# Kernel tuning notes

Hardware: AMD Instinct MI355X
Metric: run time of the kernel (lower is better)

## Reference

```python
import jax, jax.numpy as jnp
import numpy as np
import math

B, M, DM = 4, 4096, 1024
H, HD = 16, 64            # head_dim = hidden_dim // num_heads
SEG, DIL = 128, 2         # segment_size, dilation_rate
BLOCK_M = 64              # kernel query-block size (min(64, M))
SCALE = HD ** -0.5


def _hilbert_map(seq_len):
    # Faithful port of create_hilbert_mapping_fixed (boustrophedon scan).
    if seq_len <= 64:
        return np.arange(seq_len, dtype=np.int32)
    g = int(math.ceil(math.sqrt(seq_len)))
    mp = np.zeros(seq_len, dtype=np.int64)
    idx = 0
    for row in range(g):
        cols = range(g) if row % 2 == 0 else range(g - 1, -1, -1)
        for col in cols:
            if idx < seq_len:
                lp = row * g + col
                if lp < seq_len:
                    mp[lp] = idx
                    idx += 1
    for i in range(seq_len):
        if i >= idx:
            mp[i] = i
    return mp.astype(np.int32)


def setup_inputs() -> dict:
    key = jax.random.key(0)
    k1, k2, k3 = jax.random.split(key, 3)
    x = jax.random.normal(k1, (B, M, DM), jnp.float32)
    Wqkv = jax.random.normal(k2, (3 * DM, DM), jnp.float32) * 0.02
    Wout = jax.random.normal(k3, (DM, DM), jnp.float32) * 0.02
    hmap = jnp.asarray(_hilbert_map(M))
    return {"x": x, "Wqkv": Wqkv, "Wout": Wout, "hmap": hmap}


def _hilbert_attention(x, Wqkv, Wout, hmap):
    Bn, Mn, _ = x.shape
    qkv = x @ Wqkv.T                                   # [B,M,3*DM]
    qkv = qkv.reshape(Bn, Mn, 3, H, HD).transpose(2, 0, 3, 1, 4)
    q, k, v = qkv[0], qkv[1], qkv[2]                   # [B,H,M,HD]

    S = Mn // SEG           # number of segments
    T = SEG // DIL          # keys per segment (dilated offsets 0, DIL, 2*DIL, ...)
    NB = SEG // BLOCK_M     # query blocks per segment

    # Queries gathered through Hilbert map, pre-scaled (as in kernel).
    qh = q[:, :, hmap, :] * SCALE                      # [B,H,M,HD]

    # Dilated key positions per segment, gathered through Hilbert map.
    key_pos = (jnp.arange(S)[:, None] * SEG + jnp.arange(T)[None, :] * DIL).reshape(-1)
    kh = k[:, :, hmap[key_pos], :].reshape(Bn, H, S, T, HD)
    vh = v[:, :, hmap[key_pos], :].reshape(Bn, H, S, T, HD)

    # Scores per (query-block within segment, key): [B,H,S,NB,BLOCK_M,T]
    qs = qh.reshape(Bn, H, S, NB, BLOCK_M, HD)
    scores = jnp.einsum('bhsnqd,bhstd->bhsnqt', qs, kh)

    # Kernel quirk (faithful): per-KEY max taken over the 64-query block,
    # exp accumulated without rescaling -> NOT a true softmax.
    c = jnp.max(scores, axis=4, keepdims=True)         # max over query block
    w = jnp.exp(scores - c)
    num = jnp.einsum('bhsnqt,bhstd->bhsnqd', w, vh)
    den = 1e-10 + jnp.sum(w, axis=-1, keepdims=True)
    out = (num / den).reshape(Bn, H, Mn, HD)

    # Stored at linear (non-Hilbert) positions, then merged heads + out proj.
    out = out.transpose(0, 2, 1, 3).reshape(Bn, Mn, H * HD)
    return out @ Wout.T


def reference(x, Wqkv, Wout, hmap):
    return _hilbert_attention(x, Wqkv, Wout, hmap)
```

## Files before the change

kernel.cpp:

```cpp
#include <hip/hip_runtime.h>
#include <hip/hip_bf16.h>

#define BB 4
#define MM 4096
#define DM 1024
#define NH 16
#define HDIM 64
#define SEGSZ 128
#define NSEG 32
#define ROWS (BB*MM)
#define QKVC (3*DM)
#define KVROWS (BB*MM/2)
#define KVLD 2048
#define NX4  (ROWS*DM/4)
#define NW14 (QKVC*DM/4)
#define NW24 (DM*DM/4)

typedef __attribute__((ext_vector_type(8))) short bf16x8;
typedef __attribute__((ext_vector_type(4))) float f32x4;

__device__ inline unsigned short f2bf(float f) {
  __hip_bfloat16 h = __float2bfloat16(f);
  return *reinterpret_cast<unsigned short*>(&h);
}

__device__ __forceinline__ void gld16(const ushort* g, ushort* l) {
  __builtin_amdgcn_global_load_lds(
      (const __attribute__((address_space(1))) unsigned int*)g,
      (__attribute__((address_space(3))) unsigned int*)l,
      16, 0, 0);
}

__global__ __launch_bounds__(256) void cvt_all(const float4* __restrict__ x,
                                               const float4* __restrict__ w1,
                                               const float4* __restrict__ w2,
                                               ushort4* __restrict__ xo,
                                               ushort4* __restrict__ w1o,
                                               ushort4* __restrict__ w2o) {
  int i = blockIdx.x * 256 + threadIdx.x;
  const float4* src; ushort4* dst; int off;
  if (i < NX4)              { src = x;  dst = xo;  off = i; }
  else if (i < NX4 + NW14)  { src = w1; dst = w1o; off = i - NX4; }
  else                      { src = w2; dst = w2o; off = i - NX4 - NW14; }
  float4 v = src[off];
  ushort4 o;
  o.x = f2bf(v.x); o.y = f2bf(v.y); o.z = f2bf(v.z); o.w = f2bf(v.w);
  dst[off] = o;
}

__global__ __launch_bounds__(256) void gemm_qkv(const ushort* __restrict__ xbf,
                                                const ushort* __restrict__ wqkv,
                                                ushort* __restrict__ qhb,
                                                ushort* __restrict__ kvb,
                                                const int* __restrict__ hmap) {
  __shared__ __align__(16) ushort sA[128 * 32];
  __shared__ __align__(16) ushort sB[128 * 32];
  __shared__ int sRow[128];
  const int blk = blockIdx.x;
  const int tid = threadIdx.x;
  const int lane = tid & 63;
  const int wave = tid >> 6;
  const int m16 = lane & 15;
  const int quad = lane >> 4;

  const ushort* Bmat; ushort* C; int row0, col0, N;
  if (blk < 1024) {
    row0 = (blk >> 3) * 128; col0 = (blk & 7) * 128;
    Bmat = wqkv; C = qhb; N = DM;
  } else {
    int j = blk - 1024;
    row0 = (j >> 4) * 128; col0 = (j & 15) * 128;
    Bmat = wqkv + (size_t)DM * DM; C = kvb; N = KVLD;
  }

  if (tid < 128) {
    int m = row0 + tid, xrow;
    if (blk < 1024) {
      int b = m >> 12, p = m & 4095;
      xrow = (b << 12) + hmap[p];
    } else {
      int b = m >> 11, idx = m & 2047;
      int s = idx >> 6, t = idx & 63;
      xrow = (b << 12) + hmap[s * SEGSZ + 2 * t];
    }
    sRow[tid] = xrow;
  }
  __syncthreads();

  f32x4 acc[4][4] = {};
  const int wr = (wave >> 1) * 64;
  const int wc = (wave & 1) * 64;

  const int ch0 = wave * 64 + lane;
  const int ch1 = 256 + wave * 64 + lane;
  const int r0 = ch0 >> 2, k0 = (ch0 & 3) * 8;
  const int r1 = ch1 >> 2, k1 = (ch1 & 3) * 8;

  const ushort* pa0 = xbf + (size_t)sRow[r0] * DM + k0;
  const ushort* pa1 = xbf + (size_t)sRow[r1] * DM + k1;
  const ushort* pb0 = Bmat + (size_t)(col0 + r0) * DM + k0;
  const ushort* pb1 = Bmat + (size_t)(col0 + r1) * DM + k1;
  ushort* sA0 = sA + wave * 512;
  ushort* sA1 = sA + 2048 + wave * 512;
  ushort* sB0 = sB + wave * 512;
  ushort* sB1 = sB + 2048 + wave * 512;

  for (int kt = 0; kt < DM; kt += 32) {
    __syncthreads();
    gld16(pa0 + kt, sA0);
    gld16(pa1 + kt, sA1);
    gld16(pb0 + kt, sB0);
    gld16(pb1 + kt, sB1);
    __syncthreads();

    bf16x8 af[4], bfr[4];
#pragma unroll
    for (int i = 0; i < 4; ++i) {
      af[i]  = *(const bf16x8*)(sA + (wr + i * 16 + m16) * 32 + quad * 8);
      bfr[i] = *(const bf16x8*)(sB + (wc + i * 16 + m16) * 32 + quad * 8);
    }
#pragma unroll
    for (int i = 0; i < 4; ++i)
#pragma unroll
      for (int j = 0; j < 4; ++j)
        acc[i][j] = __builtin_amdgcn_mfma_f32_16x16x32_bf16(af[i], bfr[j], acc[i][j], 0, 0, 0);
  }

#pragma unroll
  for (int i = 0; i < 4; ++i)
#pragma unroll
    for (int r = 0; r < 4; ++r) {
      int row = row0 + wr + i * 16 + quad * 4 + r;
#pragma unroll
      for (int j = 0; j < 4; ++j)
        C[(size_t)row * N + col0 + wc + j * 16 + m16] = f2bf(acc[i][j][r]);
    }
}

__global__ __launch_bounds__(256) void gemm_out(const ushort* __restrict__ A,
                                                const ushort* __restrict__ Bmat,
                                                float* __restrict__ C) {
  __shared__ __align__(16) ushort sA[128 * 32];
  __shared__ __align__(16) ushort sB[64 * 32];
  const int blk = blockIdx.x;
  const int row0 = (blk >> 4) * 128;
  const int col0 = (blk & 15) * 64;
  const int tid = threadIdx.x;
  const int lane = tid & 63;
  const int wave = tid >> 6;
  const int m16 = lane & 15;
  const int quad = lane >> 4;
  const int wr = (wave >> 1) * 64;
  const int wc = (wave & 1) * 32;

  f32x4 acc[4][2] = {};

  const int ch0 = wave * 64 + lane;
  const int ch1 = 256 + wave * 64 + lane;
  const int ra0 = ch0 >> 2, ka0 = (ch0 & 3) * 8;
  const int ra1 = ch1 >> 2, ka1 = (ch1 & 3) * 8;

  const ushort* pa0 = A + (size_t)(row0 + ra0) * DM + ka0;
  const ushort* pa1 = A + (size_t)(row0 + ra1) * DM + ka1;
  const ushort* pb0 = Bmat + (size_t)(col0 + ra0) * DM + ka0;
  ushort* lA0 = sA + wave * 512;
  ushort* lA1 = sA + 2048 + wave * 512;
  ushort* lB0 = sB + wave * 512;

  for (int kt = 0; kt < DM; kt += 32) {
    __syncthreads();
    gld16(pa0 + kt, lA0);
    gld16(pa1 + kt, lA1);
    gld16(pb0 + kt, lB0);
    __syncthreads();

    bf16x8 af[4], bfr[2];
#pragma unroll
    for (int i = 0; i < 4; ++i)
      af[i] = *(const bf16x8*)(sA + (wr + i * 16 + m16) * 32 + quad * 8);
#pragma unroll
    for (int j = 0; j < 2; ++j)
      bfr[j] = *(const bf16x8*)(sB + (wc + j * 16 + m16) * 32 + quad * 8);
#pragma unroll
    for (int i = 0; i < 4; ++i)
#pragma unroll
      for (int j = 0; j < 2; ++j)
        acc[i][j] = __builtin_amdgcn_mfma_f32_16x16x32_bf16(af[i], bfr[j], acc[i][j], 0, 0, 0);
  }

#pragma unroll
  for (int i = 0; i < 4; ++i)
#pragma unroll
    for (int r = 0; r < 4; ++r) {
      int row = row0 + wr + i * 16 + quad * 4 + r;
#pragma unroll
      for (int j = 0; j < 2; ++j)
        C[(size_t)row * DM + col0 + wc + j * 16 + m16] = acc[i][j][r];
    }
}

__global__ __launch_bounds__(256) void attn_kernel(const ushort* __restrict__ qh,
                                                   const ushort* __restrict__ kv,
                                                   ushort* __restrict__ out) {
  __shared__ __align__(16) ushort sQW[128 * 72];
  __shared__ __align__(16) ushort sK[64 * 72];
  __shared__ __align__(16) ushort sVT[64 * 72];
  __shared__ float sCmaxW[4 * 64];
  __shared__ float sDen[128];

  const int bid = blockIdx.x;
  const int s  = bid & 31;
  const int h  = (bid >> 5) & 15;
  const int b  = bid >> 9;
  const int tid = threadIdx.x;
  const int lane = tid & 63;
  const int wave = tid >> 6;
  const int m16 = lane & 15;
  const int quad = lane >> 4;
  const int qb = wave * 32;
  const int hb = wave >> 1;

  {
    const int qr = tid >> 1;
    const int qc = (tid & 1) * 32;
    const ushort* qrow = qh + (size_t)(b * MM + s * SEGSZ + qr) * DM + h * HDIM + qc;
    *(uint4*)(sQW + qr * 72 + qc)      = ((const uint4*)qrow)[0];
    *(uint4*)(sQW + qr * 72 + qc + 8)  = ((const uint4*)qrow)[1];
    *(uint4*)(sQW + qr * 72 + qc + 16) = ((const uint4*)qrow)[2];
    *(uint4*)(sQW + qr * 72 + qc + 24) = ((const uint4*)qrow)[3];

    const int r = tid >> 2;
    const int c = (tid & 3) * 16;
    const ushort* krow = kv + (size_t)(b * (MM/2) + s * 64 + r) * KVLD + h * HDIM + c;
    const ushort* vrow = krow + DM;
    *(uint4*)(sK + r * 72 + c)     = ((const uint4*)krow)[0];
    *(uint4*)(sK + r * 72 + c + 8) = ((const uint4*)krow)[1];
    ushort vv[16];
    *(uint4*)(vv)     = ((const uint4*)vrow)[0];
    *(uint4*)(vv + 8) = ((const uint4*)vrow)[1];
#pragma unroll
    for (int u = 0; u < 16; ++u) sVT[(c + u) * 72 + r] = vv[u];
  }
  __syncthreads();

  f32x4 sc[2][4];
  {
    bf16x8 aq[2][2], bk[4][2];
#pragma unroll
    for (int ks = 0; ks < 2; ++ks) {
#pragma unroll
      for (int ib = 0; ib < 2; ++ib)
        aq[ib][ks] = *(const bf16x8*)(sQW + (qb + ib * 16 + m16) * 72 + ks * 32 + quad * 8);
#pragma unroll
      for (int j = 0; j < 4; ++j)
        bk[j][ks] = *(const bf16x8*)(sK + (j * 16 + m16) * 72 + ks * 32 + quad * 8);
    }
#pragma unroll
    for (int ib = 0; ib < 2; ++ib)
#pragma unroll
      for (int j = 0; j < 4; ++j) {
        f32x4 a = {};
        a = __builtin_amdgcn_mfma_f32_16x16x32_bf16(aq[ib][0], bk[j][0], a, 0, 0, 0);
        a = __builtin_amdgcn_mfma_f32_16x16x32_bf16(aq[ib][1], bk[j][1], a, 0, 0, 0);
        sc[ib][j] = a * 0.125f;
      }
  }

#pragma unroll
  for (int j = 0; j < 4; ++j) {
    float m = -1e30f;
#pragma unroll
    for (int ib = 0; ib < 2; ++ib)
#pragma unroll
      for (int r = 0; r < 4; ++r) m = fmaxf(m, sc[ib][j][r]);
    m = fmaxf(m, __shfl_xor(m, 16));
    m = fmaxf(m, __shfl_xor(m, 32));
    if (quad == 0) sCmaxW[wave * 64 + j * 16 + m16] = m;
  }
  __syncthreads();

  {
    float part[2][4] = {};
#pragma unroll
    for (int j = 0; j < 4; ++j) {
      const int col = j * 16 + m16;
      float c0 = fmaxf(sCmaxW[hb * 128 + col], sCmaxW[hb * 128 + 64 + col]);
#pragma unroll
      for (int ib = 0; ib < 2; ++ib)
#pragma unroll
        for (int r = 0; r < 4; ++r) {
          float ww = __expf(sc[ib][j][r] - c0);
          sc[ib][j][r] = ww;
          part[ib][r] += ww;
        }
    }
#pragma unroll
    for (int ib = 0; ib < 2; ++ib)
#pragma unroll
      for (int r = 0; r < 4; ++r) {
        float p = part[ib][r];
        p += __shfl_xor(p, 1); p += __shfl_xor(p, 2);
        p += __shfl_xor(p, 4); p += __shfl_xor(p, 8);
        if (m16 == 0) sDen[qb + ib * 16 + quad * 4 + r] = p;
      }
#pragma unroll
    for (int ib = 0; ib < 2; ++ib)
#pragma unroll
      for (int j = 0; j < 4; ++j)
#pragma unroll
        for (int r = 0; r < 4; ++r)
          sQW[(qb + ib * 16 + quad * 4 + r) * 72 + j * 16 + m16] = f2bf(sc[ib][j][r]);
  }
  __syncthreads();

  f32x4 o[2][4] = {};
  {
    bf16x8 aw[2][2], bv[4][2];
#pragma unroll
    for (int ks = 0; ks < 2; ++ks) {
#pragma unroll
      for (int ib = 0; ib < 2; ++ib)
        aw[ib][ks] = *(const bf16x8*)(sQW + (qb + ib * 16 + m16) * 72 + ks * 32 + quad * 8);
#pragma unroll
      for (int j = 0; j < 4; ++j)
        bv[j][ks] = *(const bf16x8*)(sVT + (j * 16 + m16) * 72 + ks * 32 + quad * 8);
    }
#pragma unroll
    for (int ib = 0; ib < 2; ++ib)
#pragma unroll
      for (int j = 0; j < 4; ++j) {
        o[ib][j] = __builtin_amdgcn_mfma_f32_16x16x32_bf16(aw[ib][0], bv[j][0], o[ib][j], 0, 0, 0);
        o[ib][j] = __builtin_amdgcn_mfma_f32_16x16x32_bf16(aw[ib][1], bv[j][1], o[ib][j], 0, 0, 0);
      }
  }

#pragma unroll
  for (int ib = 0; ib < 2; ++ib)
#pragma unroll
    for (int r = 0; r < 4; ++r) {
      const int lrow = qb + ib * 16 + quad * 4 + r;
      float rd = 1.0f / (1e-10f + sDen[lrow]);
      ushort* op = out + (size_t)(b * MM + s * SEGSZ + lrow) * DM + h * HDIM + m16;
#pragma unroll
      for (int j = 0; j < 4; ++j)
        op[j * 16] = f2bf(o[ib][j][r] * rd);
    }
}

extern "C" void kernel_launch(void* const* d_in, const int* in_sizes, int n_in,
                              void* d_out, int out_size, void* d_ws, size_t ws_size,
                              hipStream_t stream) {
  const float* x    = (const float*)d_in[0];
  const float* wqkv = (const float*)d_in[1];
  const float* wout = (const float*)d_in[2];
  const int*   hmap = (const int*)d_in[3];
  float* outp = (float*)d_out;

  ushort* xbf    = (ushort*)d_ws;
  ushort* wqkvbf = xbf + (size_t)ROWS * DM;
  ushort* woutbf = wqkvbf + (size_t)QKVC * DM;
  ushort* qhb    = woutbf + (size_t)DM * DM;
  ushort* kvb    = qhb + (size_t)ROWS * DM;
  ushort* attn   = kvb + (size_t)KVROWS * KVLD;

  cvt_all<<<(NX4 + NW14 + NW24 + 255) / 256, 256, 0, stream>>>(
      (const float4*)x, (const float4*)wqkv, (const float4*)wout,
      (ushort4*)xbf, (ushort4*)wqkvbf, (ushort4*)woutbf);

  gemm_qkv<<<2048, 256, 0, stream>>>(xbf, wqkvbf, qhb, kvb, hmap);

  attn_kernel<<<BB * NH * NSEG, 256, 0, stream>>>(qhb, kvb, attn);

  gemm_out<<<2048, 256, 0, stream>>>(attn, woutbf, outp);
}
```

Measured before the change: 296.7 us.

## Rewrite QKV GEMM with 256x256 tiles, swizzled LDS and multi-stage pipelined loads

The QKV projection GEMM moves from 128x128 tiles with 256 threads to 256x256 tiles with 512 threads (8 waves). Global-to-LDS loads are spread over a 4-buffer ring using explicit vmcnt waits, so loads overlap MFMA work. The LDS layout is XOR-swizzled to avoid bank conflicts, and s_setprio is raised around the MFMA bursts. The aim is more data reuse per tile and hidden memory latency, at the cost of 128KB of LDS (one block per CU) and a larger grid quantum, which gives fewer blocks (512) for load balance.

```diff
diff --git a/kernel.cpp b/kernel.cpp
--- a/kernel.cpp
+++ b/kernel.cpp
@@ -48,92 +48,147 @@
   dst[off] = o;
 }
 
-__global__ __launch_bounds__(256) void gemm_qkv(const ushort* __restrict__ xbf,
+__global__ __launch_bounds__(512) void gemm_qkv(const ushort* __restrict__ xbf,
                                                 const ushort* __restrict__ wqkv,
                                                 ushort* __restrict__ qhb,
                                                 ushort* __restrict__ kvb,
                                                 const int* __restrict__ hmap) {
-  __shared__ __align__(16) ushort sA[128 * 32];
-  __shared__ __align__(16) ushort sB[128 * 32];
-  __shared__ int sRow[128];
+  __shared__ __align__(16) ushort sAB[65536];
+  __shared__ int sRow[256];
+
   const int blk = blockIdx.x;
   const int tid = threadIdx.x;
   const int lane = tid & 63;
   const int wave = tid >> 6;
   const int m16 = lane & 15;
   const int quad = lane >> 4;
+  const int wm = wave >> 2;
+  const int wn = wave & 3;
 
   const ushort* Bmat; ushort* C; int row0, col0, N;
-  if (blk < 1024) {
-    row0 = (blk >> 3) * 128; col0 = (blk & 7) * 128;
+  if (blk < 256) {
+    row0 = (blk >> 2) * 256; col0 = (blk & 3) * 256;
     Bmat = wqkv; C = qhb; N = DM;
   } else {
-    int j = blk - 1024;
-    row0 = (j >> 4) * 128; col0 = (j & 15) * 128;
+    int j = blk - 256;
+    row0 = (j >> 3) * 256; col0 = (j & 7) * 256;
     Bmat = wqkv + (size_t)DM * DM; C = kvb; N = KVLD;
   }
 
-  if (tid < 128) {
+  if (tid < 256) {
     int m = row0 + tid, xrow;
-    if (blk < 1024) {
+    if (blk < 256) {
       int b = m >> 12, p = m & 4095;
       xrow = (b << 12) + hmap[p];
     } else {
       int b = m >> 11, idx = m & 2047;
-      int s = idx >> 6, t = idx & 63;
-      xrow = (b << 12) + hmap[s * SEGSZ + 2 * t];
+      int ss = idx >> 6, tt = idx & 63;
+      xrow = (b << 12) + hmap[ss * SEGSZ + 2 * tt];
     }
     sRow[tid] = xrow;
   }
   __syncthreads();
 
-  f32x4 acc[4][4] = {};
-  const int wr = (wave >> 1) * 64;
-  const int wc = (wave & 1) * 64;
-
-  const int ch0 = wave * 64 + lane;
-  const int ch1 = 256 + wave * 64 + lane;
-  const int r0 = ch0 >> 2, k0 = (ch0 & 3) * 8;
-  const int r1 = ch1 >> 2, k1 = (ch1 & 3) * 8;
-
-  const ushort* pa0 = xbf + (size_t)sRow[r0] * DM + k0;
-  const ushort* pa1 = xbf + (size_t)sRow[r1] * DM + k1;
-  const ushort* pb0 = Bmat + (size_t)(col0 + r0) * DM + k0;
-  const ushort* pb1 = Bmat + (size_t)(col0 + r1) * DM + k1;
-  ushort* sA0 = sA + wave * 512;
-  ushort* sA1 = sA + 2048 + wave * 512;
-  ushort* sB0 = sB + wave * 512;
-  ushort* sB1 = sB + 2048 + wave * 512;
-
-  for (int kt = 0; kt < DM; kt += 32) {
-    __syncthreads();
-    gld16(pa0 + kt, sA0);
-    gld16(pa1 + kt, sA1);
-    gld16(pb0 + kt, sB0);
-    gld16(pb1 + kt, sB1);
-    __syncthreads();
-
-    bf16x8 af[4], bfr[4];
-#pragma unroll
-    for (int i = 0; i < 4; ++i) {
-      af[i]  = *(const bf16x8*)(sA + (wr + i * 16 + m16) * 32 + quad * 8);
-      bfr[i] = *(const bf16x8*)(sB + (wc + i * 16 + m16) * 32 + quad * 8);
-    }
-#pragma unroll
-    for (int i = 0; i < 4; ++i)
-#pragma unroll
-      for (int j = 0; j < 4; ++j)
-        acc[i][j] = __builtin_amdgcn_mfma_f32_16x16x32_bf16(af[i], bfr[j], acc[i][j], 0, 0, 0);
-  }
-
-#pragma unroll
-  for (int i = 0; i < 4; ++i)
-#pragma unroll
-    for (int r = 0; r < 4; ++r) {
-      int row = row0 + wr + i * 16 + quad * 4 + r;
-#pragma unroll
-      for (int j = 0; j < 4; ++j)
-        C[(size_t)row * N + col0 + wc + j * 16 + m16] = f2bf(acc[i][j][r]);
+  const int f0 = wave * 64 + lane, f1 = 512 + f0;
+  const int r0 = f0 >> 2, c0 = (f0 & 3) ^ ((f0 >> 3) & 3);
+  const int r1 = f1 >> 2, c1 = (f1 & 3) ^ ((f1 >> 3) & 3);
+  const ushort* pA0 = xbf + (size_t)sRow[r0] * DM + c0 * 8;
+  const ushort* pA1 = xbf + (size_t)sRow[r1] * DM + c1 * 8;
+  const ushort* pB0 = Bmat + (size_t)(col0 + r0) * DM + c0 * 8;
+  const ushort* pB1 = Bmat + (size_t)(col0 + r1) * DM + c1 * 8;
+
+  f32x4 acc[8][4] = {};
+
+#define STAGE_A(T, KH, DB) do {                                              \
+    gld16(pA0 + (T) * 64 + (KH) * 32,                                        \
+          sAB + ((DB) * 2 + (KH)) * 8192 + wave * 512);                      \
+    gld16(pA1 + (T) * 64 + (KH) * 32,                                        \
+          sAB + ((DB) * 2 + (KH)) * 8192 + 4096 + wave * 512);               \
+  } while (0)
+#define STAGE_B(T, KH, DB) do {                                              \
+    gld16(pB0 + (T) * 64 + (KH) * 32,                                        \
+          sAB + 32768 + ((DB) * 2 + (KH)) * 8192 + wave * 512);              \
+    gld16(pB1 + (T) * 64 + (KH) * 32,                                        \
+          sAB + 32768 + ((DB) * 2 + (KH)) * 8192 + 4096 + wave * 512);       \
+  } while (0)
+#define VM6 asm volatile("s_waitcnt vmcnt(6)" ::: "memory")
+#define VM8 asm volatile("s_waitcnt vmcnt(8)" ::: "memory")
+#define VM0 asm volatile("s_waitcnt vmcnt(0)" ::: "memory")
+#define NOPS ((void)0)
+
+#define PH(TB, KH, CH, STAGE, VMA) do {                                      \
+    const ushort* Ab = sAB + ((TB) * 2 + (KH)) * 8192;                       \
+    const ushort* Bb = sAB + 32768 + ((TB) * 2 + (KH)) * 8192;               \
+    bf16x8 af[8], bfv[2];                                                    \
+    _Pragma("unroll")                                                        \
+    for (int mf = 0; mf < 8; ++mf) {                                         \
+      int r = wm * 128 + mf * 16 + m16;                                      \
+      af[mf] = *(const bf16x8*)(Ab + r * 32 + ((quad ^ ((r >> 1) & 3)) << 3)); \
+    }                                                                        \
+    _Pragma("unroll")                                                        \
+    for (int nf = 0; nf < 2; ++nf) {                                         \
+      int r = wn * 64 + (CH) * 32 + nf * 16 + m16;                           \
+      bfv[nf] = *(const bf16x8*)(Bb + r * 32 + ((quad ^ ((r >> 1) & 3)) << 3)); \
+    }                                                                        \
+    STAGE;                                                                   \
+    VMA;                                                                     \
+    __builtin_amdgcn_s_barrier();                                            \
+    asm volatile("s_waitcnt lgkmcnt(0)" ::: "memory");                       \
+    __builtin_amdgcn_sched_barrier(0);                                       \
+    __builtin_amdgcn_s_setprio(1);                                           \
+    _Pragma("unroll")                                                        \
+    for (int mf = 0; mf < 8; ++mf)                                           \
+      _Pragma("unroll")                                                      \
+      for (int nf = 0; nf < 2; ++nf)                                         \
+        acc[mf][(CH) * 2 + nf] = __builtin_amdgcn_mfma_f32_16x16x32_bf16(    \
+            af[mf], bfv[nf], acc[mf][(CH) * 2 + nf], 0, 0, 0);               \
+    __builtin_amdgcn_s_setprio(0);                                           \
+    __builtin_amdgcn_s_barrier();                                            \
+  } while (0)
+
+  STAGE_A(0, 0, 0); STAGE_B(0, 0, 0);
+  STAGE_A(0, 1, 0); STAGE_B(0, 1, 0);
+  STAGE_A(1, 0, 1); STAGE_B(1, 0, 1);
+  VM8;
+  __builtin_amdgcn_s_barrier();
+
+#pragma unroll 1
+  for (int i = 0; i < 7; ++i) {
+    const int t1 = 2 * i + 1, t2 = 2 * i + 2, t3 = 2 * i + 3;
+    PH(0, 0, 0, STAGE_A(t1, 1, 1), NOPS);
+    PH(0, 0, 1, STAGE_B(t1, 1, 1), VM6);
+    PH(0, 1, 0, STAGE_A(t2, 0, 0), NOPS);
+    PH(0, 1, 1, STAGE_B(t2, 0, 0), VM6);
+    PH(1, 0, 0, STAGE_A(t2, 1, 0), NOPS);
+    PH(1, 0, 1, STAGE_B(t2, 1, 0), VM6);
+    PH(1, 1, 0, STAGE_A(t3, 0, 1), NOPS);
+    PH(1, 1, 1, STAGE_B(t3, 0, 1), VM6);
+  }
+  PH(0, 0, 0, STAGE_A(15, 1, 1), NOPS);
+  PH(0, 0, 1, STAGE_B(15, 1, 1), VM0);
+  PH(0, 1, 0, NOPS, NOPS);
+  PH(0, 1, 1, NOPS, NOPS);
+  PH(1, 0, 0, NOPS, NOPS);
+  PH(1, 0, 1, NOPS, NOPS);
+  PH(1, 1, 0, NOPS, NOPS);
+  PH(1, 1, 1, NOPS, NOPS);
+
+#undef PH
+#undef STAGE_A
+#undef STAGE_B
+#undef VM6
+#undef VM8
+#undef VM0
+#undef NOPS
+
+#pragma unroll
+  for (int mf = 0; mf < 8; ++mf)
+#pragma unroll
+    for (int rr = 0; rr < 4; ++rr) {
+      int row = row0 + wm * 128 + mf * 16 + quad * 4 + rr;
+#pragma unroll
+      for (int nf = 0; nf < 4; ++nf)
+        C[(size_t)row * N + col0 + wn * 64 + nf * 16 + m16] = f2bf(acc[mf][nf][rr]);
     }
 }
 
@@ -367,7 +422,7 @@
       (const float4*)x, (const float4*)wqkv, (const float4*)wout,
       (ushort4*)xbf, (ushort4*)wqkvbf, (ushort4*)woutbf);
 
-  gemm_qkv<<<2048, 256, 0, stream>>>(xbf, wqkvbf, qhb, kvb, hmap);
+  gemm_qkv<<<512, 512, 0, stream>>>(xbf, wqkvbf, qhb, kvb, hmap);
 
   attn_kernel<<<BB * NH * NSEG, 256, 0, stream>>>(qhb, kvb, attn);
 
```

Measured after the change: 293.2 us. No clear change (-1.2%).
